# Performance work log

Hardware: AMD Instinct MI355X
Metric: run time of the kernel (lower is better)

Reference implementation:

```python
import jax, jax.numpy as jnp
import numpy as np

V, E, U, B, S = 32000, 512, 1024, 4, 2048


def setup_inputs() -> dict:
    key = jax.random.key(0)
    k = jax.random.split(key, 7)
    inputs = jax.random.randint(k[0], (B, S), 0, V, dtype=jnp.int32)
    emb = jax.random.normal(k[1], (V, E), dtype=jnp.float32) * 0.02
    Wx = jax.random.normal(k[2], (E, 3 * U), dtype=jnp.float32) / np.sqrt(E)
    Wh = jax.random.normal(k[3], (U, 3 * U), dtype=jnp.float32) / np.sqrt(U)
    bx = jnp.zeros((3 * U,), dtype=jnp.float32)
    bh = jnp.zeros((3 * U,), dtype=jnp.float32)
    Wd = jax.random.normal(k[4], (U, V), dtype=jnp.float32) / np.sqrt(U)
    bd = jnp.zeros((V,), dtype=jnp.float32)
    return {"inputs": inputs, "emb": emb, "Wx": Wx, "Wh": Wh,
            "bx": bx, "bh": bh, "Wd": Wd, "bd": bd}


def _gru_seq(x, Wx, Wh, bx, bh):
    # x: [B,S,E] -> hidden states [B,S,U]. Keras GRU, reset_after=True.
    xg = jnp.einsum('bse,eu->bsu', x, Wx) + bx  # [B,S,3U], input gates precomputed

    def step(h, xg_t):
        hg = h @ Wh + bh                      # [B,3U]
        xz, xr, xh = jnp.split(xg_t, 3, axis=-1)
        hz, hr, hh = jnp.split(hg, 3, axis=-1)
        z = jax.nn.sigmoid(xz + hz)
        r = jax.nn.sigmoid(xr + hr)
        hc = jnp.tanh(xh + r * hh)
        h_new = z * h + (1.0 - z) * hc
        return h_new, h_new

    h0 = jnp.zeros((x.shape[0], Wh.shape[0]), dtype=x.dtype)
    _, hs = jax.lax.scan(step, h0, jnp.swapaxes(xg, 0, 1))  # time-major scan
    return jnp.swapaxes(hs, 0, 1)  # [B,S,U]


def reference(inputs, emb, Wx, Wh, bx, bh, Wd, bd):
    x = emb[inputs]                      # [B,S,E] embedding lookup
    hs = _gru_seq(x, Wx, Wh, bx, bh)     # [B,S,U]
    logits = jnp.einsum('bsu,uv->bsv', hs, Wd) + bd  # [B,S,V]
    return logits
```

## Files before the change

### kernel.cpp

```cpp
#include <hip/hip_runtime.h>
#include <hip/hip_bf16.h>
#include <cstdint>
#include <cstddef>

#define V_SZ 32000
#define E_SZ 512
#define U_SZ 1024
#define B_SZ 4
#define S_SZ 2048
#define NGRU 128
#define NTILES 16000
#define GRID_FUSED 256

typedef _Float16 f16;
typedef _Float16 f16x2 __attribute__((ext_vector_type(2)));
typedef _Float16 f16x8 __attribute__((ext_vector_type(8)));
typedef _Float16 f16x4 __attribute__((ext_vector_type(4)));
typedef float    f32x4 __attribute__((ext_vector_type(4)));
typedef unsigned long long u64;

__device__ __forceinline__ void async_copy16(const void* g, void* l) {
  __builtin_amdgcn_global_load_lds(
      (const __attribute__((address_space(1))) void*)g,
      (__attribute__((address_space(3))) void*)l, 16, 0, 0);
}

__device__ __forceinline__ f32x4 mfma16(f16x8 a, f16x8 b, f32x4 c) {
  return __builtin_amdgcn_mfma_f32_16x16x32_f16(a, b, c, 0, 0, 0);
}

__device__ __forceinline__ float wave_sum64(float v) {
  v += __int_as_float(__builtin_amdgcn_update_dpp(0, __float_as_int(v), 0x111, 0xf, 0xf, true));
  v += __int_as_float(__builtin_amdgcn_update_dpp(0, __float_as_int(v), 0x112, 0xf, 0xf, true));
  v += __int_as_float(__builtin_amdgcn_update_dpp(0, __float_as_int(v), 0x114, 0xf, 0xf, true));
  v += __int_as_float(__builtin_amdgcn_update_dpp(0, __float_as_int(v), 0x118, 0xf, 0xf, true));
  v += __int_as_float(__builtin_amdgcn_update_dpp(0, __float_as_int(v), 0x142, 0xa, 0xf, true));
  v += __int_as_float(__builtin_amdgcn_update_dpp(0, __float_as_int(v), 0x143, 0xc, 0xf, true));
  return v;
}

__global__ void k_gather_split(const int* __restrict__ inputs, const float* __restrict__ emb,
                               f16* __restrict__ x_hi, f16* __restrict__ x_lo) {
  int m = blockIdx.x;
  int row = inputs[m];
  const float* src = emb + (size_t)row * E_SZ;
  int j = threadIdx.x * 4;
  f32x4 v = *(const f32x4*)(src + j);
  f16x4 hi, lo;
#pragma unroll
  for (int q = 0; q < 4; ++q) {
    f16 h = (f16)v[q];
    hi[q] = h;
    lo[q] = (f16)((v[q] - (float)h) * 4096.0f);
  }
  *(f16x4*)(x_hi + (size_t)m * E_SZ + j) = hi;
  *(f16x4*)(x_lo + (size_t)m * E_SZ + j) = lo;
}

__global__ void k_transpose_split(const float* __restrict__ W, f16* __restrict__ Wt,
                                  int K, int N) {
  __shared__ float tile[32][33];
  int tx = threadIdx.x & 31, ty = threadIdx.x >> 5;
  int n0 = blockIdx.x * 32, k0 = blockIdx.y * 32;
#pragma unroll
  for (int i = 0; i < 4; ++i)
    tile[ty + 8 * i][tx] = W[(size_t)(k0 + ty + 8 * i) * N + n0 + tx];
  __syncthreads();
#pragma unroll
  for (int i = 0; i < 4; ++i)
    Wt[(size_t)(n0 + ty + 8 * i) * K + k0 + tx] = (f16)tile[tx][ty + 8 * i];
}

template<int K, bool REMAP>
__global__ __launch_bounds__(256, 2)
void k_gemm2s(const f16* __restrict__ Ah, const f16* __restrict__ Al,
              const f16* __restrict__ Bt, const float* __restrict__ bias,
              float* __restrict__ C, int N) {
  __shared__ f16 lds[2][3 * 4096];
  const int tid = threadIdx.x;
  const int lane = tid & 63;
  const int wave = tid >> 6;
  const int wm = wave >> 1, wn = wave & 1;
  const int m0 = blockIdx.y * 128;
  const int n0 = blockIdx.x * 128;

  auto stage = [&](int buf, int kk) {
#pragma unroll
    for (int i = 0; i < 6; ++i) {
      int g = i * 256 + tid;
      int tile = g >> 9;
      int idx = g & 511;
      int r = idx >> 2;
      int kg = (idx & 3) ^ ((r >> 1) & 3);
      const f16* src = (tile == 0) ? Ah : (tile == 1) ? Al : Bt;
      int row = (tile == 2) ? (n0 + r) : (m0 + r);
      const f16* gp = src + (size_t)row * K + kk + kg * 8;
      f16* lp = &lds[buf][(g & ~63) * 8];
      async_copy16(gp, lp);
    }
  };

  f32x4 accH[4][4] = {};
  f32x4 accL[4][4] = {};
  stage(0, 0);
  int buf = 0;
  for (int kk = 0; kk < K; kk += 32) {
    __syncthreads();
    if (kk + 32 < K) stage(buf ^ 1, kk + 32);
    const f16* base = &lds[buf][0];
    const int kg = lane >> 4;
    f16x8 bfr[4];
#pragma unroll
    for (int fn = 0; fn < 4; ++fn) {
      int r = wn * 64 + fn * 16 + (lane & 15);
      bfr[fn] = *(const f16x8*)(base + 2 * 4096 + r * 32 + ((kg ^ ((r >> 1) & 3)) * 8));
    }
#pragma unroll
    for (int fm = 0; fm < 4; ++fm) {
      int r = wm * 64 + fm * 16 + (lane & 15);
      int off = r * 32 + ((kg ^ ((r >> 1) & 3)) * 8);
      f16x8 ah = *(const f16x8*)(base + off);
      f16x8 al = *(const f16x8*)(base + 4096 + off);
#pragma unroll
      for (int fn = 0; fn < 4; ++fn) {
        accH[fm][fn] = mfma16(ah, bfr[fn], accH[fm][fn]);
        accL[fm][fn] = mfma16(al, bfr[fn], accL[fm][fn]);
      }
    }
    buf ^= 1;
  }
  const float inv = 1.0f / 4096.0f;
#pragma unroll
  for (int fn = 0; fn < 4; ++fn) {
    int col = n0 + wn * 64 + fn * 16 + (lane & 15);
    float bv = bias[col];
#pragma unroll
    for (int fm = 0; fm < 4; ++fm) {
      int row0 = m0 + wm * 64 + fm * 16 + ((lane >> 4) << 2);
#pragma unroll
      for (int j = 0; j < 4; ++j) {
        int row = row0 + j;
        float v = accH[fm][fn][j] + inv * accL[fm][fn][j] + bv;
        size_t orow = REMAP ? ((size_t)(row & (S_SZ - 1)) * B_SZ + (row >> 11))
                            : (size_t)row;
        C[orow * (size_t)N + col] = v;
      }
    }
  }
}


__device__ __forceinline__ void gru_role(int role, char* smem,
    const float* __restrict__ xg, const float* __restrict__ Wh,
    const float* __restrict__ bh, u64* __restrict__ h_ring,
    f16* __restrict__ hs_hi, f16* __restrict__ hs_lo, unsigned* __restrict__ cnt) {
  float (*Whs)[1028] = (float(*)[1028])smem;
  const int tid = threadIdx.x;
  const int lane = tid & 63;
  const int wave = tid >> 6;
  const int u0 = role * 8;
  const int col0 = u0 + wave * 2;

  f32x4 Wreg[6][4];
  for (int gate = 0; gate < 3; ++gate) {
    __syncthreads();
    for (int idx = tid; idx < 8 * 1024; idx += 256) {
      int j = idx & 7, k = idx >> 3;
      Whs[j][k] = Wh[(size_t)k * 3072 + gate * 1024 + u0 + j];
    }
    __syncthreads();
#pragma unroll
    for (int cj = 0; cj < 2; ++cj)
#pragma unroll
      for (int i = 0; i < 4; ++i)
        Wreg[gate * 2 + cj][i] = *(const f32x4*)&Whs[wave * 2 + cj][i * 256 + lane * 4];
  }
  __builtin_amdgcn_s_setprio(1);

  const float bz0 = bh[col0],        bz1 = bh[col0 + 1];
  const float br0 = bh[1024 + col0], br1 = bh[1024 + col0 + 1];
  const float bq0 = bh[2048 + col0], bq1 = bh[2048 + col0 + 1];
  float hold0[4] = {0.f, 0.f, 0.f, 0.f};
  float hold1[4] = {0.f, 0.f, 0.f, 0.f};
  const u64 POIS = 0xFFFFFFFFFFFFFFFFull;

  u64 q[8];
  const u64* pbase;
  auto pollLoads = [&]() {
#pragma unroll
    for (int i = 0; i < 4; ++i) {
      q[2 * i]     = __hip_atomic_load(pbase + i * 128 + 2 * lane,
                                       __ATOMIC_RELAXED, __HIP_MEMORY_SCOPE_AGENT);
      q[2 * i + 1] = __hip_atomic_load(pbase + i * 128 + 2 * lane + 1,
                                       __ATOMIC_RELAXED, __HIP_MEMORY_SCOPE_AGENT);
    }
  };
  auto issue = [&](int slot, int row) {
    pbase = h_ring + ((size_t)slot * B_SZ + row) * 512;
    pollLoads();
  };
  float2 xzv[4], xrv[4], xhv[4];
  auto xgIssue = [&](int b2, int t2) {
    const float* p = xg + ((size_t)t2 * B_SZ + b2) * 3072 + col0;
    xzv[b2] = *(const float2*)p;
    xrv[b2] = *(const float2*)(p + 1024);
    xhv[b2] = *(const float2*)(p + 2048);
  };

  issue(0, 0);
  xgIssue(0, 0); xgIssue(1, 0); xgIssue(2, 0); xgIssue(3, 0);

  for (int t = 0; t < S_SZ; ++t) {
#pragma unroll
    for (int b = 0; b < 4; ++b) {
      const float2 xz = xzv[b], xr = xrv[b], xh = xhv[b];
      {
        bool ok = (q[0] != POIS) && (q[1] != POIS) && (q[2] != POIS) && (q[3] != POIS)
               && (q[4] != POIS) && (q[5] != POIS) && (q[6] != POIS) && (q[7] != POIS);
        if (!__all(ok)) {
          while (true) {
            __builtin_amdgcn_s_sleep(1);
            pollLoads();
            bool ok2 = (q[0] != POIS) && (q[1] != POIS) && (q[2] != POIS) && (q[3] != POIS)
                    && (q[4] != POIS) && (q[5] != POIS) && (q[6] != POIS) && (q[7] != POIS);
            if (__all(ok2)) break;
          }
        }
      }
      float hp[16];
#pragma unroll
      for (int j2 = 0; j2 < 8; ++j2) {
        hp[2 * j2]     = __uint_as_float((unsigned int)q[j2]);
        hp[2 * j2 + 1] = __uint_as_float((unsigned int)(q[j2] >> 32));
      }
      float a6[6];
#pragma unroll
      for (int c = 0; c < 6; ++c) {
        float v = 0.0f;
#pragma unroll
        for (int i = 0; i < 4; ++i)
#pragma unroll
          for (int qq = 0; qq < 4; ++qq)
            v += Wreg[c][i][qq] * hp[4 * i + qq];
        a6[c] = v;
      }
      float s0 = wave_sum64(a6[0]), s1 = wave_sum64(a6[1]), s2 = wave_sum64(a6[2]);
      float s3 = wave_sum64(a6[3]), s4 = wave_sum64(a6[4]), s5 = wave_sum64(a6[5]);

      asm volatile("" ::: "memory");
      {
        const int nb = (b + 1) & 3;
        const int nt = (b == 3) ? (t + 1) : t;
        issue(nt & 7, nb);
        const int tp1 = (t + 1 < S_SZ) ? (t + 1) : (S_SZ - 1);
        xgIssue(b, tp1);
      }
      asm volatile("" ::: "memory");

      if (lane == 63) {
        __hip_atomic_store(h_ring + ((size_t)((t + 4) & 7) * B_SZ + b) * 512 + (col0 >> 1),
                           POIS, __ATOMIC_RELAXED, __HIP_MEMORY_SCOPE_AGENT);
        float z0 = __builtin_amdgcn_rcpf(1.0f + __expf(-(xz.x + s0 + bz0)));
        float z1 = __builtin_amdgcn_rcpf(1.0f + __expf(-(xz.y + s1 + bz1)));
        float r0 = __builtin_amdgcn_rcpf(1.0f + __expf(-(xr.x + s2 + br0)));
        float r1 = __builtin_amdgcn_rcpf(1.0f + __expf(-(xr.y + s3 + br1)));
        float a0 = xh.x + r0 * (s4 + bq0);
        float a1 = xh.y + r1 * (s5 + bq1);
        float e0 = __expf(-2.0f * fabsf(a0));
        float e1 = __expf(-2.0f * fabsf(a1));
        float hc0 = copysignf((1.0f - e0) * __builtin_amdgcn_rcpf(1.0f + e0), a0);
        float hc1 = copysignf((1.0f - e1) * __builtin_amdgcn_rcpf(1.0f + e1), a1);
        float h0 = z0 * hold0[b] + (1.0f - z0) * hc0;
        float h1 = z1 * hold1[b] + (1.0f - z1) * hc1;
        hold0[b] = h0; hold1[b] = h1;
        u64 hv = ((u64)__float_as_uint(h1) << 32) | (u64)__float_as_uint(h0);
        __hip_atomic_store(h_ring + ((size_t)((t + 1) & 7) * B_SZ + b) * 512 + (col0 >> 1),
                           hv, __ATOMIC_RELAXED, __HIP_MEMORY_SCOPE_AGENT);
        size_t hidx = ((size_t)b * S_SZ + t) * U_SZ + col0;
        f16 h0h = (f16)h0, h1h = (f16)h1;
        f16x2 hi2; hi2[0] = h0h; hi2[1] = h1h;
        f16x2 lo2;
        lo2[0] = (f16)((h0 - (float)h0h) * 4096.0f);
        lo2[1] = (f16)((h1 - (float)h1h) * 4096.0f);
        unsigned uhi, ulo;
        __builtin_memcpy(&uhi, &hi2, 4);
        __builtin_memcpy(&ulo, &lo2, 4);
        __hip_atomic_store((unsigned*)(hs_hi + hidx), uhi,
                           __ATOMIC_RELAXED, __HIP_MEMORY_SCOPE_AGENT);
        __hip_atomic_store((unsigned*)(hs_lo + hidx), ulo,
                           __ATOMIC_RELAXED, __HIP_MEMORY_SCOPE_AGENT);
        if ((t & 127) == 127) {
          asm volatile("s_waitcnt vmcnt(0)" ::: "memory");
          __hip_atomic_fetch_add(&cnt[(((unsigned)t >> 7) << 2) | (unsigned)b], 1u,
                                 __ATOMIC_RELAXED, __HIP_MEMORY_SCOPE_AGENT);
        }
      }
    }
  }
}

__device__ __forceinline__ void gemm_role(char* smem, int* sh_tile,
    const f16* __restrict__ Ah, const f16* __restrict__ Al,
    const f16* __restrict__ Bt, const float* __restrict__ bd,
    float* __restrict__ out, unsigned* __restrict__ cnt, unsigned* __restrict__ ttix) {
  f16 (*lds)[3 * 4096] = (f16(*)[3 * 4096])smem;
  const int tid = threadIdx.x;
  const int lane = tid & 63;
  const int wave = tid >> 6;
  const int wm = wave >> 1, wn = wave & 1;

  for (;;) {
    __syncthreads();
    if (tid == 0)
      *sh_tile = (int)__hip_atomic_fetch_add(ttix, 1u, __ATOMIC_RELAXED,
                                             __HIP_MEMORY_SCOPE_AGENT);
    __syncthreads();
    const int tile = *sh_tile;
    if (tile >= NTILES) break;
    const int g = tile / 250;
    const int n0 = (tile % 250) * 128;
    if (tid == 0) {
      while (__hip_atomic_load(&cnt[g], __ATOMIC_RELAXED, __HIP_MEMORY_SCOPE_AGENT) < 512u)
        __builtin_amdgcn_s_sleep(10);
    }
    __syncthreads();
    const int m0 = (g & 3) * S_SZ + (g >> 2) * 128;

    f32x4 accH[4][4] = {};
    f32x4 accL[4][4] = {};
    f32x4 areg[4];
    auto issueA = [&](int kk) {
#pragma unroll
      for (int i = 0; i < 4; ++i) {
        int gg = i * 256 + tid;
        int idx = gg & 511, r = idx >> 2;
        int kg = (idx & 3) ^ ((r >> 1) & 3);
        const f16* src = (gg >> 9) ? Al : Ah;
        const f16* gp = src + (size_t)(m0 + r) * 1024 + kk + kg * 8;
        asm volatile("global_load_dwordx4 %0, %1, off sc0 sc1"
                     : "=&v"(areg[i]) : "v"(gp) : "memory");
      }
    };
    auto issueB = [&](int buf, int kk) {
#pragma unroll
      for (int i = 4; i < 6; ++i) {
        int gg = i * 256 + tid;
        int idx = gg & 511, r = idx >> 2;
        int kg = (idx & 3) ^ ((r >> 1) & 3);
        const f16* gp = Bt + (size_t)(n0 + r) * 1024 + kk + kg * 8;
        f16* lp = &lds[buf][(gg & ~63) * 8];
        async_copy16(gp, lp);
      }
    };
    auto writeA = [&](int buf) {
#pragma unroll
      for (int i = 0; i < 4; ++i) {
        int gg = i * 256 + tid;
        *(f32x4*)&lds[buf][gg * 8] = areg[i];
      }
    };

    issueA(0); issueB(0, 0);
    asm volatile("s_waitcnt vmcnt(2)" ::: "memory");
    writeA(0);
    int buf = 0;
    for (int kk = 0; kk < 1024; kk += 32) {
      __syncthreads();
      const bool more = (kk + 32 < 1024);
      if (more) { issueA(kk + 32); issueB(buf ^ 1, kk + 32); }
      const f16* base = &lds[buf][0];
      const int kgl = lane >> 4;
      f16x8 bfr[4];
#pragma unroll
      for (int fn = 0; fn < 4; ++fn) {
        int r = wn * 64 + fn * 16 + (lane & 15);
        bfr[fn] = *(const f16x8*)(base + 2 * 4096 + r * 32 + ((kgl ^ ((r >> 1) & 3)) * 8));
      }
#pragma unroll
      for (int fm = 0; fm < 4; ++fm) {
        int r = wm * 64 + fm * 16 + (lane & 15);
        int off = r * 32 + ((kgl ^ ((r >> 1) & 3)) * 8);
        f16x8 ah = *(const f16x8*)(base + off);
        f16x8 al = *(const f16x8*)(base + 4096 + off);
#pragma unroll
        for (int fn = 0; fn < 4; ++fn) {
          accH[fm][fn] = mfma16(ah, bfr[fn], accH[fm][fn]);
          accL[fm][fn] = mfma16(al, bfr[fn], accL[fm][fn]);
        }
      }
      if (more) {
        asm volatile("s_waitcnt vmcnt(2)" ::: "memory");
        writeA(buf ^ 1);
      }
      buf ^= 1;
    }
    const float inv = 1.0f / 4096.0f;
#pragma unroll
    for (int fn = 0; fn < 4; ++fn) {
      int col = n0 + wn * 64 + fn * 16 + (lane & 15);
      float bv = bd[col];
#pragma unroll
      for (int fm = 0; fm < 4; ++fm) {
        int row0 = m0 + wm * 64 + fm * 16 + ((lane >> 4) << 2);
#pragma unroll
        for (int j = 0; j < 4; ++j) {
          float v = accH[fm][fn][j] + inv * accL[fm][fn][j] + bv;
          float* p = out + (size_t)(row0 + j) * V_SZ + col;
          asm volatile("global_store_dword %0, %1, off nt" :: "v"(p), "v"(v) : "memory");
        }
      }
    }
  }
}

__global__ __launch_bounds__(256, 1)
void k_fused(const float* __restrict__ xg, const float* __restrict__ Wh,
             const float* __restrict__ bh, u64* __restrict__ h_ring,
             f16* __restrict__ hs_hi, f16* __restrict__ hs_lo,
             const f16* __restrict__ Wd_t, const float* __restrict__ bd,
             float* __restrict__ out, unsigned* __restrict__ cnt,
             unsigned* __restrict__ tix) {
  __shared__ __align__(16) char smem[49152];
  __shared__ int sh_role;
  __shared__ int sh_tile;
  if (threadIdx.x == 0)
    sh_role = (int)__hip_atomic_fetch_add(&tix[0], 1u, __ATOMIC_RELAXED,
                                          __HIP_MEMORY_SCOPE_AGENT);
  __syncthreads();
  const int role = sh_role;
  if (role < NGRU)
    gru_role(role, smem, xg, Wh, bh, h_ring, hs_hi, hs_lo, cnt);
  else
    gemm_role(smem, &sh_tile, hs_hi, hs_lo, Wd_t, bd, out, cnt, &tix[1]);
}

extern "C" void kernel_launch(void* const* d_in, const int* in_sizes, int n_in,
                              void* d_out, int out_size, void* d_ws, size_t ws_size,
                              hipStream_t stream) {
  const int*   inputs = (const int*)d_in[0];
  const float* emb    = (const float*)d_in[1];
  const float* Wx     = (const float*)d_in[2];
  const float* Wh     = (const float*)d_in[3];
  const float* bx     = (const float*)d_in[4];
  const float* bh     = (const float*)d_in[5];
  const float* Wd     = (const float*)d_in[6];
  const float* bd     = (const float*)d_in[7];
  float* out = (float*)d_out;

  char* ws = (char*)d_ws;
  f16*   x_hi  = (f16*)(ws + 0);
  f16*   x_lo  = (f16*)(ws + 8388608);
  f16*   Wx_t  = (f16*)(ws + 16777216);
  f16*   Wd_t  = (f16*)(ws + 19922944);
  f16*   hs_hi = (f16*)(ws + 85458944);
  f16*   hs_lo = (f16*)(ws + 102236160);
  float* xg    = (float*)(ws + 119013376);
  u64*   h_ring = (u64*)(ws + 219676672);
  unsigned* cnt = (unsigned*)(ws + 219807744);
  unsigned* tix = (unsigned*)(ws + 219808000);

  hipMemsetAsync(ws + 219676672, 0x00, 16384, stream);
  hipMemsetAsync(ws + 219676672 + 16384, 0xFF, 114688, stream);
  hipMemsetAsync(ws + 219807744, 0x00, 512, stream);

  k_gather_split<<<B_SZ * S_SZ, 128, 0, stream>>>(inputs, emb, x_hi, x_lo);
  k_transpose_split<<<dim3(3072 / 32, 512 / 32), 256, 0, stream>>>(Wx, Wx_t, 512, 3072);
  k_transpose_split<<<dim3(V_SZ / 32, 1024 / 32), 256, 0, stream>>>(Wd, Wd_t, 1024, V_SZ);
  k_gemm2s<512, true><<<dim3(3072 / 128, 8192 / 128), 256, 0, stream>>>(
      x_hi, x_lo, Wx_t, bx, xg, 3072);
  k_fused<<<GRID_FUSED, 256, 0, stream>>>(xg, Wh, bh, h_ring, hs_hi, hs_lo,
                                          Wd_t, bd, out, cnt, tix);
}
```

Measured before the change: 8.954 ms.

## Batch GRU recurrence polling across all four batch rows per timestep

The recurrent step used to poll one batch row's hidden state at a time and prefetch the next row in a rolling pipeline. It now loads all four rows of the ring slot at once, waits for all of them together, computes all four matvec reductions, then prefetches the next timestep's slot before the lane-63 gate math. The xg loads move to lane 63 only and are no longer prefetched a step ahead. This cuts per-row poll round trips, at the cost of more registers (32 u64 values) and waiting for the slowest of the four rows.

Result: slower. 20.71 ms (+131.3%).

```diff
diff --git a/kernel.cpp b/kernel.cpp
--- a/kernel.cpp
+++ b/kernel.cpp
@@ -184,56 +184,62 @@
   float hold1[4] = {0.f, 0.f, 0.f, 0.f};
   const u64 POIS = 0xFFFFFFFFFFFFFFFFull;
 
-  u64 q[8];
-  const u64* pbase;
-  auto pollLoads = [&]() {
-#pragma unroll
-    for (int i = 0; i < 4; ++i) {
-      q[2 * i]     = __hip_atomic_load(pbase + i * 128 + 2 * lane,
-                                       __ATOMIC_RELAXED, __HIP_MEMORY_SCOPE_AGENT);
-      q[2 * i + 1] = __hip_atomic_load(pbase + i * 128 + 2 * lane + 1,
-                                       __ATOMIC_RELAXED, __HIP_MEMORY_SCOPE_AGENT);
+  u64 q[4][8];
+  auto pollAll = [&](int slot) __attribute__((always_inline)) {
+#pragma unroll
+    for (int b = 0; b < 4; ++b) {
+      const u64* base = h_ring + ((size_t)slot * B_SZ + b) * 512 + 2 * lane;
+#pragma unroll
+      for (int i = 0; i < 4; ++i) {
+        q[b][2 * i]     = __hip_atomic_load(base + i * 128,
+                                            __ATOMIC_RELAXED, __HIP_MEMORY_SCOPE_AGENT);
+        q[b][2 * i + 1] = __hip_atomic_load(base + i * 128 + 1,
+                                            __ATOMIC_RELAXED, __HIP_MEMORY_SCOPE_AGENT);
+      }
     }
   };
-  auto issue = [&](int slot, int row) {
-    pbase = h_ring + ((size_t)slot * B_SZ + row) * 512;
-    pollLoads();
-  };
-  float2 xzv[4], xrv[4], xhv[4];
-  auto xgIssue = [&](int b2, int t2) {
-    const float* p = xg + ((size_t)t2 * B_SZ + b2) * 3072 + col0;
-    xzv[b2] = *(const float2*)p;
-    xrv[b2] = *(const float2*)(p + 1024);
-    xhv[b2] = *(const float2*)(p + 2048);
-  };
-
-  issue(0, 0);
-  xgIssue(0, 0); xgIssue(1, 0); xgIssue(2, 0); xgIssue(3, 0);
+
+  pollAll(0);
 
   for (int t = 0; t < S_SZ; ++t) {
+    float2 xz[4], xr[4], xh[4];
+    if (lane == 63) {
+#pragma unroll
+      for (int b = 0; b < 4; ++b) {
+        const float* p = xg + ((size_t)t * B_SZ + b) * 3072 + col0;
+        xz[b] = *(const float2*)p;
+        xr[b] = *(const float2*)(p + 1024);
+        xh[b] = *(const float2*)(p + 2048);
+      }
+    }
+    {
+      bool ok = true;
+#pragma unroll
+      for (int b = 0; b < 4; ++b)
+#pragma unroll
+        for (int i = 0; i < 8; ++i) ok = ok && (q[b][i] != POIS);
+      if (!__all(ok)) {
+        while (true) {
+          __builtin_amdgcn_s_sleep(1);
+          pollAll(t & 7);
+          bool ok2 = true;
+#pragma unroll
+          for (int b = 0; b < 4; ++b)
+#pragma unroll
+            for (int i = 0; i < 8; ++i) ok2 = ok2 && (q[b][i] != POIS);
+          if (__all(ok2)) break;
+        }
+      }
+    }
+    float sred[4][6];
 #pragma unroll
     for (int b = 0; b < 4; ++b) {
-      const float2 xz = xzv[b], xr = xrv[b], xh = xhv[b];
-      {
-        bool ok = (q[0] != POIS) && (q[1] != POIS) && (q[2] != POIS) && (q[3] != POIS)
-               && (q[4] != POIS) && (q[5] != POIS) && (q[6] != POIS) && (q[7] != POIS);
-        if (!__all(ok)) {
-          while (true) {
-            __builtin_amdgcn_s_sleep(1);
-            pollLoads();
-            bool ok2 = (q[0] != POIS) && (q[1] != POIS) && (q[2] != POIS) && (q[3] != POIS)
-                    && (q[4] != POIS) && (q[5] != POIS) && (q[6] != POIS) && (q[7] != POIS);
-            if (__all(ok2)) break;
-          }
-        }
-      }
       float hp[16];
 #pragma unroll
       for (int j2 = 0; j2 < 8; ++j2) {
-        hp[2 * j2]     = __uint_as_float((unsigned int)q[j2]);
-        hp[2 * j2 + 1] = __uint_as_float((unsigned int)(q[j2] >> 32));
-      }
-      float a6[6];
+        hp[2 * j2]     = __uint_as_float((unsigned int)q[b][j2]);
+        hp[2 * j2 + 1] = __uint_as_float((unsigned int)(q[b][j2] >> 32));
+      }
 #pragma unroll
       for (int c = 0; c < 6; ++c) {
         float v = 0.0f;
@@ -242,30 +248,23 @@
 #pragma unroll
           for (int qq = 0; qq < 4; ++qq)
             v += Wreg[c][i][qq] * hp[4 * i + qq];
-        a6[c] = v;
-      }
-      float s0 = wave_sum64(a6[0]), s1 = wave_sum64(a6[1]), s2 = wave_sum64(a6[2]);
-      float s3 = wave_sum64(a6[3]), s4 = wave_sum64(a6[4]), s5 = wave_sum64(a6[5]);
-
-      asm volatile("" ::: "memory");
-      {
-        const int nb = (b + 1) & 3;
-        const int nt = (b == 3) ? (t + 1) : t;
-        issue(nt & 7, nb);
-        const int tp1 = (t + 1 < S_SZ) ? (t + 1) : (S_SZ - 1);
-        xgIssue(b, tp1);
-      }
-      asm volatile("" ::: "memory");
-
-      if (lane == 63) {
+        sred[b][c] = wave_sum64(v);
+      }
+    }
+    asm volatile("" ::: "memory");
+    pollAll((t + 1) & 7);
+    asm volatile("" ::: "memory");
+    if (lane == 63) {
+#pragma unroll
+      for (int b = 0; b < 4; ++b) {
         __hip_atomic_store(h_ring + ((size_t)((t + 4) & 7) * B_SZ + b) * 512 + (col0 >> 1),
                            POIS, __ATOMIC_RELAXED, __HIP_MEMORY_SCOPE_AGENT);
-        float z0 = __builtin_amdgcn_rcpf(1.0f + __expf(-(xz.x + s0 + bz0)));
-        float z1 = __builtin_amdgcn_rcpf(1.0f + __expf(-(xz.y + s1 + bz1)));
-        float r0 = __builtin_amdgcn_rcpf(1.0f + __expf(-(xr.x + s2 + br0)));
-        float r1 = __builtin_amdgcn_rcpf(1.0f + __expf(-(xr.y + s3 + br1)));
-        float a0 = xh.x + r0 * (s4 + bq0);
-        float a1 = xh.y + r1 * (s5 + bq1);
+        float z0 = __builtin_amdgcn_rcpf(1.0f + __expf(-(xz[b].x + sred[b][0] + bz0)));
+        float z1 = __builtin_amdgcn_rcpf(1.0f + __expf(-(xz[b].y + sred[b][1] + bz1)));
+        float r0 = __builtin_amdgcn_rcpf(1.0f + __expf(-(xr[b].x + sred[b][2] + br0)));
+        float r1 = __builtin_amdgcn_rcpf(1.0f + __expf(-(xr[b].y + sred[b][3] + br1)));
+        float a0 = xh[b].x + r0 * (sred[b][4] + bq0);
+        float a1 = xh[b].y + r1 * (sred[b][5] + bq1);
         float e0 = __expf(-2.0f * fabsf(a0));
         float e1 = __expf(-2.0f * fabsf(a1));
         float hc0 = copysignf((1.0f - e0) * __builtin_amdgcn_rcpf(1.0f + e0), a0);
@@ -289,11 +288,13 @@
                            __ATOMIC_RELAXED, __HIP_MEMORY_SCOPE_AGENT);
         __hip_atomic_store((unsigned*)(hs_lo + hidx), ulo,
                            __ATOMIC_RELAXED, __HIP_MEMORY_SCOPE_AGENT);
-        if ((t & 127) == 127) {
-          asm volatile("s_waitcnt vmcnt(0)" ::: "memory");
+      }
+      if ((t & 127) == 127) {
+        asm volatile("s_waitcnt vmcnt(0)" ::: "memory");
+#pragma unroll
+        for (int b = 0; b < 4; ++b)
           __hip_atomic_fetch_add(&cnt[(((unsigned)t >> 7) << 2) | (unsigned)b], 1u,
                                  __ATOMIC_RELAXED, __HIP_MEMORY_SCOPE_AGENT);
-        }
       }
     }
   }
```
